# Optimization experiments

Hardware: AMD Instinct MI355X
Metric: run time of the kernel (lower is better)

## Reference

```python
import jax, jax.numpy as jnp
import numpy as np

BLOCK = 128  # fp8 block-quant block size (128, 128)


def dequant_block_fp8_weight(w, scale_inv):
    """w: [O, I] fp8-valued weights (stored as f32); scale_inv: [O//128, I//128].
    Dequant = per-(128,128)-block multiply by scale."""
    O, I = w.shape
    wb = w.reshape(O // BLOCK, BLOCK, I // BLOCK, BLOCK)
    wb = wb * scale_inv[:, None, :, None]
    return wb.reshape(O, I)


def setup_inputs() -> dict:
    key = jax.random.key(0)
    ks = jax.random.split(key, 7)
    H, F, T = 5120, 1536, 8192  # hidden, moe_intermediate, tokens
    x = jax.random.normal(ks[0], (T, H), dtype=jnp.float32)
    w_gate = jax.random.normal(ks[1], (F, H), dtype=jnp.float32)
    s_gate = jax.random.uniform(ks[2], (F // BLOCK, H // BLOCK), dtype=jnp.float32) * 0.01 + 1e-4
    w_up = jax.random.normal(ks[3], (F, H), dtype=jnp.float32)
    s_up = jax.random.uniform(ks[4], (F // BLOCK, H // BLOCK), dtype=jnp.float32) * 0.01 + 1e-4
    w_down = jax.random.normal(ks[5], (H, F), dtype=jnp.float32)
    s_down = jax.random.uniform(ks[6], (H // BLOCK, F // BLOCK), dtype=jnp.float32) * 0.01 + 1e-4
    return {"x": x, "w_gate": w_gate, "s_gate": s_gate, "w_up": w_up,
            "s_up": s_up, "w_down": w_down, "s_down": s_down}


def reference(x, w_gate, s_gate, w_up, s_up, w_down, s_down):
    # down_proj(silu(gate_proj(x)) * up_proj(x)), each Linear dequantizing
    # block-scaled fp8 weights first (bias=False everywhere).
    wg = dequant_block_fp8_weight(w_gate, s_gate).astype(x.dtype)
    wu = dequant_block_fp8_weight(w_up, s_up).astype(x.dtype)
    wd = dequant_block_fp8_weight(w_down, s_down).astype(x.dtype)
    gate = jnp.einsum('th,fh->tf', x, wg)  # [T, F]
    up = jnp.einsum('th,fh->tf', x, wu)    # [T, F]
    h = jax.nn.silu(gate) * up
    out = jnp.einsum('tf,hf->th', h, wd)   # [T, H]
    return out
```

## Files before the change

kernel.cpp:

```cpp
#include <hip/hip_runtime.h>


typedef __bf16 bf16x8 __attribute__((ext_vector_type(8)));
typedef float  f32x4  __attribute__((ext_vector_type(4)));

#define BK 32

__device__ __forceinline__ void stage128x32(const __bf16* __restrict__ gbase,
                                            __bf16* lds, int ldk, int tid) {
#pragma unroll
  for (int i = 0; i < 2; ++i) {
    int c = tid + i * 256;
    int row = c >> 2;
    int q = c & 3;
    const __bf16* g = gbase + (size_t)row * ldk + q * 8;
    __builtin_amdgcn_global_load_lds(
        (const __attribute__((address_space(1))) void*)g,
        (__attribute__((address_space(3))) void*)(lds + c * 8),
        16, 0, 0);
  }
}

__device__ __forceinline__ void cast8(const float* __restrict__ in,
                                      __bf16* __restrict__ out, size_t idx) {
  f32x4 a = *(const f32x4*)(in + idx);
  f32x4 b = *(const f32x4*)(in + idx + 4);
  bf16x8 o;
#pragma unroll
  for (int i = 0; i < 4; ++i) { o[i] = (__bf16)a[i]; o[i + 4] = (__bf16)b[i]; }
  *(bf16x8*)(out + idx) = o;
}

__device__ __forceinline__ void dq_ilv(const float* __restrict__ w,
                                       const float* __restrict__ s,
                                       __bf16* __restrict__ wq, int r, int tid,
                                       int which) {
  unsigned idx = ((unsigned)r * 256u + (unsigned)tid) * 8u;
  unsigned f = idx / 5120u;
  unsigned h = idx - f * 5120u;
  float sc = s[(f >> 7) * 40 + (h >> 7)];
  f32x4 a = *(const f32x4*)(w + idx);
  f32x4 b = *(const f32x4*)(w + idx + 4);
  bf16x8 o;
#pragma unroll
  for (int i = 0; i < 4; ++i) {
    o[i] = (__bf16)(a[i] * sc);
    o[i + 4] = (__bf16)(b[i] * sc);
  }
  *(bf16x8*)(wq + (size_t)(2 * f + which) * 5120 + h) = o;
}

__device__ __forceinline__ void dq_wd(const float* __restrict__ w,
                                      const float* __restrict__ s,
                                      __bf16* __restrict__ o8, int r, int tid) {
  unsigned idx = ((unsigned)r * 256u + (unsigned)tid) * 8u;
  unsigned f = idx / 1536u;
  unsigned h = idx - f * 1536u;
  float sc = s[(f >> 7) * 12 + (h >> 7)];
  f32x4 a = *(const f32x4*)(w + idx);
  f32x4 b = *(const f32x4*)(w + idx + 4);
  bf16x8 o;
#pragma unroll
  for (int i = 0; i < 4; ++i) {
    o[i] = (__bf16)(a[i] * sc);
    o[i + 4] = (__bf16)(b[i] * sc);
  }
  *(bf16x8*)(o8 + idx) = o;
}

__global__ void prep(const float* __restrict__ x, const float* __restrict__ wg,
                     const float* __restrict__ sg, const float* __restrict__ wu,
                     const float* __restrict__ su, const float* __restrict__ wd,
                     const float* __restrict__ sd, __bf16* __restrict__ xb,
                     __bf16* __restrict__ wq, __bf16* __restrict__ wdq) {
  int bid = blockIdx.x;
  int tid = threadIdx.x;
  if (bid < 20480) {
    cast8(x, xb, ((size_t)bid * 256 + tid) * 8);
  } else if (bid < 24320) {
    dq_ilv(wg, sg, wq, bid - 20480, tid, 0);
  } else if (bid < 28160) {
    dq_ilv(wu, su, wq, bid - 24320, tid, 1);
  } else {
    dq_wd(wd, sd, wdq, bid - 28160, tid);
  }
}

template <bool FUSE_SILU, typename OutT>
__global__ void gemm_bt(const __bf16* __restrict__ A,
                        const __bf16* __restrict__ B, OutT* __restrict__ C,
                        int M, int N, int K, int ldc) {
  __shared__ __bf16 sA[128 * BK];
  __shared__ __bf16 sB[128 * BK];
  const int tid = threadIdx.x;
  const int lane = tid & 63;
  const int wave = tid >> 6;
  const int wm = (wave >> 1) * 64;
  const int wn = (wave & 1) * 64;
  const int m0 = blockIdx.y * 128;
  const int n0 = blockIdx.x * 128;
  const int lr = lane & 15;
  const int lk = (lane >> 4) * 8;

  f32x4 acc[4][4] = {};

  const __bf16* Ab = A + (size_t)m0 * K;
  const __bf16* Bb = B + (size_t)n0 * K;

  for (int k0 = 0; k0 < K; k0 += BK) {
    stage128x32(Ab + k0, sA, K, tid);
    stage128x32(Bb + k0, sB, K, tid);
    __syncthreads();
    bf16x8 af[4];
#pragma unroll
    for (int i = 0; i < 4; ++i)
      af[i] = *(const bf16x8*)(sA + (wm + i * 16 + lr) * BK + lk);
#pragma unroll
    for (int j = 0; j < 4; ++j) {
      bf16x8 bf = *(const bf16x8*)(sB + (wn + j * 16 + lr) * BK + lk);
#pragma unroll
      for (int i = 0; i < 4; ++i)
        acc[i][j] =
            __builtin_amdgcn_mfma_f32_16x16x32_bf16(af[i], bf, acc[i][j], 0, 0, 0);
    }
    __syncthreads();
  }

  const int colb = n0 + wn + lr;
  const int rowb = m0 + wm + (lane >> 4) * 4;
#pragma unroll
  for (int i = 0; i < 4; ++i)
#pragma unroll
    for (int j = 0; j < 4; ++j)
#pragma unroll
      for (int r = 0; r < 4; ++r) {
        if constexpr (FUSE_SILU) {
          float v = acc[i][j][r];
          float p = __shfl_xor(v, 1, 64);
          float g = (lane & 1) ? p : v;
          float u = (lane & 1) ? v : p;
          float hv = (g / (1.0f + __expf(-g))) * u;
          if ((lane & 1) == 0)
            C[(size_t)(rowb + i * 16 + r) * ldc + ((colb + j * 16) >> 1)] =
                (OutT)hv;
        } else {
          C[(size_t)(rowb + i * 16 + r) * ldc + (colb + j * 16)] =
              (OutT)acc[i][j][r];
        }
      }
}

extern "C" void kernel_launch(void* const* d_in, const int* in_sizes, int n_in,
                              void* d_out, int out_size, void* d_ws,
                              size_t ws_size, hipStream_t stream) {
  const int Hd = 5120, Fd = 1536, Td = 8192;
  const float* x = (const float*)d_in[0];
  const float* wg = (const float*)d_in[1];
  const float* sg = (const float*)d_in[2];
  const float* wu = (const float*)d_in[3];
  const float* su = (const float*)d_in[4];
  const float* wd = (const float*)d_in[5];
  const float* sd = (const float*)d_in[6];
  float* out = (float*)d_out;

  __bf16* ws = (__bf16*)d_ws;
  const size_t xsz = (size_t)Td * Hd;
  __bf16* xb = ws;
  __bf16* wq = xb + xsz;
  __bf16* wdq = wq + (size_t)2 * Fd * Hd;
  __bf16* hbuf = wdq + (size_t)Hd * Fd;

  prep<<<32000, 256, 0, stream>>>(x, wg, sg, wu, su, wd, sd, xb, wq, wdq);

  dim3 g1(2 * Fd / 128, Td / 128);
  gemm_bt<true, __bf16><<<g1, 256, 0, stream>>>(xb, wq, hbuf, Td, 2 * Fd, Hd,
                                                Fd);

  dim3 g2(Hd / 128, Td / 128);
  gemm_bt<false, float><<<g2, 256, 0, stream>>>(hbuf, wdq, out, Td, Hd, Fd, Hd);
}
```

Before: 811.8 us.

## Rewrite GEMM with 4-stage LDS pipeline, 128x256 tiles, swizzle, XCD remap

Replaces the single-buffered 128x128 GEMM with a 512-thread, 128x256 tile kernel. Global-to-LDS loads are staged three tiles ahead across four LDS buffers, synchronised with vmcnt-based barriers. It also adds an XOR swizzle to avoid LDS bank conflicts, a block-index remap that spreads tiles across XCDs, and raised wave priority around the MFMA section. The aim is to hide global load latency and the double __syncthreads stalls of the old loop. The cost is higher LDS use (96KB per block), which may limit occupancy.

```diff
diff --git a/kernel.cpp b/kernel.cpp
--- a/kernel.cpp
+++ b/kernel.cpp
@@ -4,22 +4,26 @@
 typedef __bf16 bf16x8 __attribute__((ext_vector_type(8)));
 typedef float  f32x4  __attribute__((ext_vector_type(4)));
 
-#define BK 32
-
-__device__ __forceinline__ void stage128x32(const __bf16* __restrict__ gbase,
-                                            __bf16* lds, int ldk, int tid) {
-#pragma unroll
-  for (int i = 0; i < 2; ++i) {
-    int c = tid + i * 256;
-    int row = c >> 2;
-    int q = c & 3;
-    const __bf16* g = gbase + (size_t)row * ldk + q * 8;
-    __builtin_amdgcn_global_load_lds(
-        (const __attribute__((address_space(1))) void*)g,
-        (__attribute__((address_space(3))) void*)(lds + c * 8),
-        16, 0, 0);
-  }
-}
+__device__ __forceinline__ void glds16(const __bf16* g, __bf16* l) {
+  __builtin_amdgcn_global_load_lds(
+      (const __attribute__((address_space(1))) void*)g,
+      (__attribute__((address_space(3))) void*)l, 16, 0, 0);
+}
+
+__device__ __forceinline__ void chunk_rk(int c, int& row, int& k) {
+  int s = c >> 6;
+  int w = (c & 63) << 4;
+  int wl = w ^ (((w >> 9) & 1) << 5) ^ (((w >> 7) & 1) << 4);
+  row = (s << 4) + (wl >> 6);
+  k = (wl & 63) >> 1;
+}
+
+#define SYNC(n)                                                        \
+  do {                                                                 \
+    __builtin_amdgcn_sched_barrier(0);                                 \
+    asm volatile("s_waitcnt vmcnt(" #n ")\n\ts_barrier" ::: "memory"); \
+    __builtin_amdgcn_sched_barrier(0);                                 \
+  } while (0)
 
 __device__ __forceinline__ void cast8(const float* __restrict__ in,
                                       __bf16* __restrict__ out, size_t idx) {
@@ -87,47 +91,82 @@
 }
 
 template <bool FUSE_SILU, typename OutT>
-__global__ void gemm_bt(const __bf16* __restrict__ A,
-                        const __bf16* __restrict__ B, OutT* __restrict__ C,
-                        int M, int N, int K, int ldc) {
-  __shared__ __bf16 sA[128 * BK];
-  __shared__ __bf16 sB[128 * BK];
+__global__ __launch_bounds__(512, 2) void gemm_p(
+    const __bf16* __restrict__ A, const __bf16* __restrict__ B,
+    OutT* __restrict__ C, int M, int N, int K, int ldc, int nbx) {
+  __shared__ __bf16 lds[4 * 12288];
   const int tid = threadIdx.x;
   const int lane = tid & 63;
   const int wave = tid >> 6;
-  const int wm = (wave >> 1) * 64;
-  const int wn = (wave & 1) * 64;
-  const int m0 = blockIdx.y * 128;
-  const int n0 = blockIdx.x * 128;
   const int lr = lane & 15;
-  const int lk = (lane >> 4) * 8;
-
-  f32x4 acc[4][4] = {};
-
+
+  const int nwg = gridDim.x;
+  const int lb = (blockIdx.x & 7) * (nwg >> 3) + (blockIdx.x >> 3);
+  const int bx = lb % nbx;
+  const int by = lb / nbx;
+  const int m0 = by * 128, n0 = bx * 256;
+
+  int laneoff = (lr << 6) | ((lane >> 4) << 4);
+  laneoff ^= ((lr & 2) << 3) | ((lr & 8) << 2);
+  const int wm4 = wave & 4;
+  const int wn4 = (wave & 3) << 2;
+
+  int ra, ka, rb0, kb0, rb1, kb1;
+  chunk_rk(tid, ra, ka);
+  chunk_rk(tid, rb0, kb0);
+  chunk_rk(tid + 512, rb1, kb1);
   const __bf16* Ab = A + (size_t)m0 * K;
   const __bf16* Bb = B + (size_t)n0 * K;
-
-  for (int k0 = 0; k0 < K; k0 += BK) {
-    stage128x32(Ab + k0, sA, K, tid);
-    stage128x32(Bb + k0, sB, K, tid);
-    __syncthreads();
-    bf16x8 af[4];
+  const unsigned offA = (unsigned)ra * K + (unsigned)ka;
+  const unsigned offB0 = (unsigned)rb0 * K + (unsigned)kb0;
+  const unsigned offB1 = (unsigned)rb1 * K + (unsigned)kb1;
+
+  f32x4 acc[4][4] = {};
+
+  auto STAGE = [&](int t, int bufi) {
+    __bf16* lb_ = lds + bufi * 12288;
+    const unsigned ko = (unsigned)t << 5;
+    glds16(Ab + (offA + ko), lb_ + (tid << 3));
+    glds16(Bb + (offB0 + ko), lb_ + 4096 + (tid << 3));
+    glds16(Bb + (offB1 + ko), lb_ + 4096 + ((tid + 512) << 3));
+  };
+  auto COMPUTE = [&](int bufi) {
+    const char* base = (const char*)lds + bufi * 24576;
+    bf16x8 af[4], bg[4];
 #pragma unroll
     for (int i = 0; i < 4; ++i)
-      af[i] = *(const bf16x8*)(sA + (wm + i * 16 + lr) * BK + lk);
-#pragma unroll
-    for (int j = 0; j < 4; ++j) {
-      bf16x8 bf = *(const bf16x8*)(sB + (wn + j * 16 + lr) * BK + lk);
+      af[i] = *(const bf16x8*)(base + ((wm4 + i) << 10) + laneoff);
+#pragma unroll
+    for (int j = 0; j < 4; ++j)
+      bg[j] = *(const bf16x8*)(base + 8192 + ((wn4 + j) << 10) + laneoff);
+    __builtin_amdgcn_s_setprio(1);
+#pragma unroll
+    for (int j = 0; j < 4; ++j)
 #pragma unroll
       for (int i = 0; i < 4; ++i)
-        acc[i][j] =
-            __builtin_amdgcn_mfma_f32_16x16x32_bf16(af[i], bf, acc[i][j], 0, 0, 0);
-    }
-    __syncthreads();
-  }
-
-  const int colb = n0 + wn + lr;
-  const int rowb = m0 + wm + (lane >> 4) * 4;
+        acc[i][j] = __builtin_amdgcn_mfma_f32_16x16x32_bf16(af[i], bg[j],
+                                                            acc[i][j], 0, 0, 0);
+    __builtin_amdgcn_s_setprio(0);
+  };
+
+  const int NT = K >> 5;
+  STAGE(0, 0);
+  STAGE(1, 1);
+  STAGE(2, 2);
+  SYNC(6);
+  int cur = 0;
+  for (int t = 0; t < NT - 3; ++t) {
+    STAGE(t + 3, (cur + 3) & 3);
+    COMPUTE(cur);
+    SYNC(6);
+    cur = (cur + 1) & 3;
+  }
+  COMPUTE(cur); SYNC(3); cur = (cur + 1) & 3;
+  COMPUTE(cur); SYNC(0); cur = (cur + 1) & 3;
+  COMPUTE(cur);
+
+  const int colb = n0 + (wn4 << 4) + lr;
+  const int rowb = m0 + (wm4 << 4) + ((lane >> 4) << 2);
 #pragma unroll
   for (int i = 0; i < 4; ++i)
 #pragma unroll
@@ -172,10 +211,9 @@
 
   prep<<<32000, 256, 0, stream>>>(x, wg, sg, wu, su, wd, sd, xb, wq, wdq);
 
-  dim3 g1(2 * Fd / 128, Td / 128);
-  gemm_bt<true, __bf16><<<g1, 256, 0, stream>>>(xb, wq, hbuf, Td, 2 * Fd, Hd,
-                                                Fd);
-
-  dim3 g2(Hd / 128, Td / 128);
-  gemm_bt<false, float><<<g2, 256, 0, stream>>>(hbuf, wdq, out, Td, Hd, Fd, Hd);
-}
+  gemm_p<true, __bf16><<<768, 512, 0, stream>>>(xb, wq, hbuf, Td, 2 * Fd, Hd,
+                                                Fd, 12);
+
+  gemm_p<false, float><<<1280, 512, 0, stream>>>(hbuf, wdq, out, Td, Hd, Fd,
+                                                 Hd, 20);
+}
```

Result: faster. 792.7 us (-2.4%).
